# Kernel optimization log

Measured on AMD Instinct MI355X. Metric: run time of the kernel, lower is better.

Reference implementation:

```python
import jax, jax.numpy as jnp
import numpy as np

BLOCK_SIZE = 256
N_EMBD = 256
HEAD_SIZE = 64


def setup_inputs() -> dict:
    key = jax.random.key(0)
    k1, k2, k3, k4, k5 = jax.random.split(key, 5)
    B, T = 256, 256
    x = jax.random.normal(k1, (B, T, N_EMBD), dtype=jnp.float32)
    # nn.Linear(n_embd, head_size, bias=False) weights, stored as [in, out] for x @ W
    s = 1.0 / np.sqrt(N_EMBD)
    Wk = jax.random.uniform(k2, (N_EMBD, HEAD_SIZE), minval=-s, maxval=s, dtype=jnp.float32)
    Wq = jax.random.uniform(k3, (N_EMBD, HEAD_SIZE), minval=-s, maxval=s, dtype=jnp.float32)
    Wv = jax.random.uniform(k4, (N_EMBD, HEAD_SIZE), minval=-s, maxval=s, dtype=jnp.float32)
    rel_pos_embedding = 0.02 * jax.random.normal(k5, (2 * BLOCK_SIZE - 1, HEAD_SIZE), dtype=jnp.float32)
    return {"x": x, "Wk": Wk, "Wq": Wq, "Wv": Wv, "rel_pos_embedding": rel_pos_embedding}


def reference(x, Wk, Wq, Wv, rel_pos_embedding):
    B, T, C = x.shape
    H = Wk.shape[-1]
    k = x @ Wk  # [B,T,H]
    q = x @ Wq  # [B,T,H]
    v = x @ Wv  # [B,T,H]
    # content scores (scaled); note: position scores are NOT scaled, matching original
    content = jnp.einsum('bth,bsh->bts', q, k) * (H ** -0.5)  # [B,T,T]
    # relative position indices: j - i + (block_size - 1)
    idx = jnp.arange(T)[None, :] - jnp.arange(T)[:, None] + (BLOCK_SIZE - 1)  # [T,T]
    rel_emb = rel_pos_embedding[idx]  # [T,T,H]
    position = jnp.einsum('bth,tsh->bts', q, rel_emb)  # [B,T,T]
    wei = content + position
    causal = jnp.tril(jnp.ones((T, T), dtype=bool))
    wei = jnp.where(causal[None, :, :], wei, -jnp.inf)
    wei = jax.nn.softmax(wei, axis=-1)
    # dropout omitted (eval mode / deterministic reference)
    out = jnp.einsum('bts,bsh->bth', wei, v)  # [B,T,H]
    return out
```

## Files before the change

kernel.cpp:

```cpp
#include <hip/hip_runtime.h>

#define BB 256
#define TT 256
#define CC 256
#define HH 64

typedef _Float16 half8 __attribute__((ext_vector_type(8)));
typedef _Float16 half4 __attribute__((ext_vector_type(4)));
typedef __fp16 fp16x2 __attribute__((ext_vector_type(2)));
typedef float floatx4 __attribute__((ext_vector_type(4)));

__global__ __launch_bounds__(256) void prep(
    const float* __restrict__ rpe,
    const float* __restrict__ Wk, const float* __restrict__ Wq, const float* __restrict__ Wv,
    _Float16* __restrict__ rpeh, _Float16* __restrict__ WT)
{
    const int bid = blockIdx.x, tid = threadIdx.x;
    if (bid < 64) {
        const int i = bid * 256 + tid;
        rpeh[i] = (_Float16)rpe[i];
    } else {
        const int wsel = (bid - 64) >> 6;
        const int n    = (bid - 64) & 63;
        const float* W = wsel == 0 ? Wk : (wsel == 1 ? Wq : Wv);
        WT[(size_t)(wsel * 64 + n) * 256 + tid] = (_Float16)W[tid * HH + n];
    }
}

__global__ __launch_bounds__(1024, 4) void fused(
    const float* __restrict__ x, const _Float16* __restrict__ WT,
    const _Float16* __restrict__ rpeh,
    _Float16* __restrict__ qh, _Float16* __restrict__ kh, _Float16* __restrict__ vTh,
    float* __restrict__ out)
{
    __shared__ __align__(16) unsigned char ldsbuf[16 * 16 * 264 * 2];
    _Float16* wt = (_Float16*)ldsbuf;

    const int tid  = threadIdx.x;
    const int b    = blockIdx.x;
    const int w    = tid >> 6;
    const int lane = tid & 63;
    const int quad = lane >> 4;
    const int l    = lane & 15;

    union H8 { half8 v; fp16x2 p[4]; };

#pragma unroll
    for (int i = tid; i < 192 * 32; i += 1024) {
        const int row = i >> 5;
        const int g   = i & 31;
        const int pg  = g ^ (row & 31);
        *(half8*)&wt[row * 256 + pg * 8] = *(const half8*)(WT + (size_t)row * 256 + g * 8);
    }
    __syncthreads();

    {
        const int row0 = b * 256 + w * 16;
        floatx4 acc[12];
#pragma unroll
        for (int nt = 0; nt < 12; ++nt) acc[nt] = (floatx4){0.f, 0.f, 0.f, 0.f};

        const float4* xg = reinterpret_cast<const float4*>(x);

#pragma unroll
        for (int kk = 0; kk < 8; ++kk) {
            const size_t base = (size_t)(row0 + l) * 64 + kk * 8 + quad * 2;
            const float4 alo = xg[base], ahi = xg[base + 1];
            H8 u;
            u.p[0] = __builtin_amdgcn_cvt_pkrtz(alo.x, alo.y);
            u.p[1] = __builtin_amdgcn_cvt_pkrtz(alo.z, alo.w);
            u.p[2] = __builtin_amdgcn_cvt_pkrtz(ahi.x, ahi.y);
            u.p[3] = __builtin_amdgcn_cvt_pkrtz(ahi.z, ahi.w);

#pragma unroll
            for (int nt = 0; nt < 12; ++nt) {
                const int row = nt * 16 + l;
                const int pg  = (kk * 4 + quad) ^ (row & 31);
                const half8 bf = *(const half8*)&wt[row * 256 + pg * 8];
                acc[nt] = __builtin_amdgcn_mfma_f32_16x16x32_f16(u.v, bf, acc[nt], 0, 0, 0);
            }
        }

        const int trw = w * 16;
#pragma unroll
        for (int nt = 0; nt < 4; ++nt) {
#pragma unroll
            for (int r = 0; r < 4; ++r) {
                const size_t row = (size_t)row0 + quad * 4 + r;
                kh[row * HH + nt * 16 + l] = (_Float16)(acc[nt][r] * 0.125f);
                qh[row * HH + nt * 16 + l] = (_Float16)acc[nt + 4][r];
            }
            half4 vv;
            vv[0] = (_Float16)acc[nt + 8][0];
            vv[1] = (_Float16)acc[nt + 8][1];
            vv[2] = (_Float16)acc[nt + 8][2];
            vv[3] = (_Float16)acc[nt + 8][3];
            *(half4*)(vTh + ((size_t)b * HH + nt * 16 + l) * TT + trw + quad * 4) = vv;
        }
    }
    __syncthreads();

    _Float16* wh = (_Float16*)ldsbuf + w * (16 * 264);
    {
        const int tile  = w;
        const int tw    = tile * 16;
        const int stmax = tile;
        const int cmax  = tile >> 1;
        const int dtmin = 15 - tile;

        const _Float16* qp = qh + (size_t)(b * TT + tw + l) * HH + quad * 8;
        const half8 qf0 = *(const half8*)qp;
        const half8 qf1 = *(const half8*)(qp + 32);

#pragma unroll
        for (int dt = 0; dt < 16; ++dt) {
            if (dt >= dtmin) {
                const _Float16* rp = rpeh + (size_t)(dt * 16 + l) * HH + quad * 8;
                const half8 bf0 = *(const half8*)rp;
                const half8 bf1 = *(const half8*)(rp + 32);
                floatx4 z = {0.f, 0.f, 0.f, 0.f};
                z = __builtin_amdgcn_mfma_f32_16x16x32_f16(qf0, bf0, z, 0, 0, 0);
                const floatx4 pacc = __builtin_amdgcn_mfma_f32_16x16x32_f16(qf1, bf1, z, 0, 0, 0);
                if (dt == dtmin) {
#pragma unroll
                    for (int r = 0; r < 4; ++r) {
                        const int row = quad * 4 + r;
                        const int s   = l + row - 15;
                        if (s >= 0) wh[row * 264 + s] = (_Float16)pacc[r];
                    }
                } else {
#pragma unroll
                    for (int r = 0; r < 4; ++r) {
                        const int row = quad * 4 + r;
                        const int s   = dt * 16 + l + tw + row - 255;
                        wh[row * 264 + s] = (_Float16)pacc[r];
                    }
                }
            }
        }

        floatx4 sacc[16];
#pragma unroll
        for (int st = 0; st < 16; ++st) {
            if (st <= stmax) {
                const _Float16* kp = kh + (size_t)(b * TT + st * 16 + l) * HH + quad * 8;
                const half8 kf0 = *(const half8*)kp;
                const half8 kf1 = *(const half8*)(kp + 32);
                floatx4 z = {0.f, 0.f, 0.f, 0.f};
                z = __builtin_amdgcn_mfma_f32_16x16x32_f16(qf0, kf0, z, 0, 0, 0);
                sacc[st] = __builtin_amdgcn_mfma_f32_16x16x32_f16(qf1, kf1, z, 0, 0, 0);
            }
        }

        float sums[4] = {0.f, 0.f, 0.f, 0.f};
#pragma unroll
        for (int st = 0; st < 16; ++st) {
            if (st < stmax) {
                const int s = l + 16 * st;
#pragma unroll
                for (int r = 0; r < 4; ++r) {
                    const int row = quad * 4 + r;
                    const float e = __expf(sacc[st][r] + (float)wh[row * 264 + s]);
                    sums[r] += e;
                    wh[row * 264 + s] = (_Float16)e;
                }
            }
        }
        {
            const int s = l + 16 * stmax;
#pragma unroll
            for (int r = 0; r < 4; ++r) {
                const int row = quad * 4 + r;
                float e = 0.f;
                if (l <= row) e = __expf(sacc[stmax][r] + (float)wh[row * 264 + s]);
                sums[r] += e;
                wh[row * 264 + s] = (_Float16)e;
            }
        }
        if ((tile & 1) == 0) {
            const int s = l + 16 * (stmax + 1);
#pragma unroll
            for (int r = 0; r < 4; ++r) wh[(quad * 4 + r) * 264 + s] = (_Float16)0.f;
        }

        float inv_r[4];
#pragma unroll
        for (int r = 0; r < 4; ++r) {
            float sum = sums[r];
            sum += __shfl_xor(sum, 1);
            sum += __shfl_xor(sum, 2);
            sum += __shfl_xor(sum, 4);
            sum += __shfl_xor(sum, 8);
            inv_r[r] = 1.0f / sum;
        }

        floatx4 oacc[4] = {{0.f,0.f,0.f,0.f},{0.f,0.f,0.f,0.f},
                           {0.f,0.f,0.f,0.f},{0.f,0.f,0.f,0.f}};
#pragma unroll
        for (int c = 0; c < 8; ++c) {
            if (c <= cmax) {
                const half8 af = *(const half8*)&wh[l * 264 + c * 32 + quad * 8];
#pragma unroll
                for (int ht = 0; ht < 4; ++ht) {
                    const half8 vf = *(const half8*)(vTh +
                        ((size_t)b * HH + ht * 16 + l) * TT + c * 32 + quad * 8);
                    oacc[ht] = __builtin_amdgcn_mfma_f32_16x16x32_f16(af, vf, oacc[ht], 0, 0, 0);
                }
            }
        }

#pragma unroll
        for (int ht = 0; ht < 4; ++ht) {
#pragma unroll
            for (int r = 0; r < 4; ++r) {
                const int t = tw + quad * 4 + r;
                out[(size_t)(b * TT + t) * HH + ht * 16 + l] = oacc[ht][r] * inv_r[r];
            }
        }
    }
}

extern "C" void kernel_launch(void* const* d_in, const int* in_sizes, int n_in,
                              void* d_out, int out_size, void* d_ws, size_t ws_size,
                              hipStream_t stream) {
    const float* x   = (const float*)d_in[0];
    const float* Wk  = (const float*)d_in[1];
    const float* Wq  = (const float*)d_in[2];
    const float* Wv  = (const float*)d_in[3];
    const float* rpe = (const float*)d_in[4];
    float* out = (float*)d_out;

    const size_t NQ = (size_t)BB * TT * HH;
    _Float16* qh   = (_Float16*)d_ws;
    _Float16* kh   = qh + NQ;
    _Float16* vTh  = kh + NQ;
    _Float16* rpeh = vTh + NQ;
    _Float16* WT   = rpeh + 256 * HH;

    prep<<<dim3(256), dim3(256), 0, stream>>>(rpe, Wk, Wq, Wv, rpeh, WT);
    fused<<<dim3(BB), dim3(1024), 0, stream>>>(x, WT, rpeh, qh, kh, vTh, out);
}
```

Baseline: 146.0 us.

## Keep K, V^T and Q in LDS instead of round-tripping through global workspace

The fused kernel no longer writes q/k/vT to a global workspace and reads them back. K and V^T now go into shared memory, and each wave passes its Q fragment through its own score slot. The weight staging is split into two 128-column halves in a pooled LDS region. That region is then reused for per-wave score buffers with triangular, variable widths, so the larger LDS footprint still fits. This removes global write and read traffic and its latency, at the cost of about 150KB of LDS per block and an extra barrier in the projection phase.

```diff
diff --git a/kernel.cpp b/kernel.cpp
--- a/kernel.cpp
+++ b/kernel.cpp
@@ -27,14 +27,25 @@
     }
 }
 
+__device__ __forceinline__ int slot_width(int w) {
+    const int j = w >> 1;
+    return (j < 2) ? 72 : (32 * j + 40);
+}
+__device__ __forceinline__ int slot_off(int w) {
+    const int j = w >> 1;
+    const int V = (j < 2) ? 72 : (32 * j + 40);
+    const int S = (j == 0) ? 0 : (j == 1) ? 72 : (16 * j * j + 24 * j + 32);
+    return 32 * S + (w & 1) * 16 * V;
+}
+
 __global__ __launch_bounds__(1024, 4) void fused(
     const float* __restrict__ x, const _Float16* __restrict__ WT,
-    const _Float16* __restrict__ rpeh,
-    _Float16* __restrict__ qh, _Float16* __restrict__ kh, _Float16* __restrict__ vTh,
-    float* __restrict__ out)
+    const _Float16* __restrict__ rpeh, float* __restrict__ out)
 {
-    __shared__ __align__(16) unsigned char ldsbuf[16 * 16 * 264 * 2];
-    _Float16* wt = (_Float16*)ldsbuf;
+    __shared__ _Float16 lds[75264];
+    _Float16* Klds = lds;
+    _Float16* VT   = lds + 18432;
+    _Float16* pool = lds + 35328;
 
     const int tid  = threadIdx.x;
     const int b    = blockIdx.x;
@@ -44,178 +55,186 @@
     const int l    = lane & 15;
 
     union H8 { half8 v; fp16x2 p[4]; };
-
-#pragma unroll
-    for (int i = tid; i < 192 * 32; i += 1024) {
-        const int row = i >> 5;
-        const int g   = i & 31;
-        const int pg  = g ^ (row & 31);
-        *(half8*)&wt[row * 256 + pg * 8] = *(const half8*)(WT + (size_t)row * 256 + g * 8);
-    }
-    __syncthreads();
+    const float4* xg = reinterpret_cast<const float4*>(x);
+    const int row0g = b * 256 + w * 16;
+
+    floatx4 acc[12];
+#pragma unroll
+    for (int nt = 0; nt < 12; ++nt) acc[nt] = (floatx4){0.f, 0.f, 0.f, 0.f};
+
+#pragma unroll
+    for (int c = 0; c < 2; ++c) {
+#pragma unroll
+        for (int i = 0; i < 3; ++i) {
+            const int gi  = tid + i * 1024;
+            const int row = gi >> 4;
+            const int g   = gi & 15;
+            *(half8*)&pool[row * 136 + g * 8] =
+                *(const half8*)(WT + (size_t)row * 256 + c * 128 + g * 8);
+        }
+        __syncthreads();
+
+        float4 xa[4][2];
+#pragma unroll
+        for (int kk = 0; kk < 4; ++kk) {
+            const size_t base = (size_t)(row0g + l) * 64 + c * 32 + kk * 8 + quad * 2;
+            xa[kk][0] = xg[base];
+            xa[kk][1] = xg[base + 1];
+        }
+#pragma unroll
+        for (int kk = 0; kk < 4; ++kk) {
+            H8 u;
+            u.p[0] = __builtin_amdgcn_cvt_pkrtz(xa[kk][0].x, xa[kk][0].y);
+            u.p[1] = __builtin_amdgcn_cvt_pkrtz(xa[kk][0].z, xa[kk][0].w);
+            u.p[2] = __builtin_amdgcn_cvt_pkrtz(xa[kk][1].x, xa[kk][1].y);
+            u.p[3] = __builtin_amdgcn_cvt_pkrtz(xa[kk][1].z, xa[kk][1].w);
+#pragma unroll
+            for (int nt = 0; nt < 12; ++nt) {
+                const half8 bf = *(const half8*)&pool[(nt * 16 + l) * 136 + kk * 32 + quad * 8];
+                acc[nt] = __builtin_amdgcn_mfma_f32_16x16x32_f16(u.v, bf, acc[nt], 0, 0, 0);
+            }
+        }
+        __syncthreads();
+    }
 
     {
-        const int row0 = b * 256 + w * 16;
-        floatx4 acc[12];
-#pragma unroll
-        for (int nt = 0; nt < 12; ++nt) acc[nt] = (floatx4){0.f, 0.f, 0.f, 0.f};
-
-        const float4* xg = reinterpret_cast<const float4*>(x);
-
-#pragma unroll
-        for (int kk = 0; kk < 8; ++kk) {
-            const size_t base = (size_t)(row0 + l) * 64 + kk * 8 + quad * 2;
-            const float4 alo = xg[base], ahi = xg[base + 1];
-            H8 u;
-            u.p[0] = __builtin_amdgcn_cvt_pkrtz(alo.x, alo.y);
-            u.p[1] = __builtin_amdgcn_cvt_pkrtz(alo.z, alo.w);
-            u.p[2] = __builtin_amdgcn_cvt_pkrtz(ahi.x, ahi.y);
-            u.p[3] = __builtin_amdgcn_cvt_pkrtz(ahi.z, ahi.w);
-
-#pragma unroll
-            for (int nt = 0; nt < 12; ++nt) {
-                const int row = nt * 16 + l;
-                const int pg  = (kk * 4 + quad) ^ (row & 31);
-                const half8 bf = *(const half8*)&wt[row * 256 + pg * 8];
-                acc[nt] = __builtin_amdgcn_mfma_f32_16x16x32_f16(u.v, bf, acc[nt], 0, 0, 0);
-            }
-        }
-
         const int trw = w * 16;
 #pragma unroll
         for (int nt = 0; nt < 4; ++nt) {
 #pragma unroll
-            for (int r = 0; r < 4; ++r) {
-                const size_t row = (size_t)row0 + quad * 4 + r;
-                kh[row * HH + nt * 16 + l] = (_Float16)(acc[nt][r] * 0.125f);
-                qh[row * HH + nt * 16 + l] = (_Float16)acc[nt + 4][r];
-            }
+            for (int r = 0; r < 4; ++r)
+                Klds[(trw + quad * 4 + r) * 72 + nt * 16 + l] = (_Float16)(acc[nt][r] * 0.125f);
             half4 vv;
             vv[0] = (_Float16)acc[nt + 8][0];
             vv[1] = (_Float16)acc[nt + 8][1];
             vv[2] = (_Float16)acc[nt + 8][2];
             vv[3] = (_Float16)acc[nt + 8][3];
-            *(half4*)(vTh + ((size_t)b * HH + nt * 16 + l) * TT + trw + quad * 4) = vv;
+            *(half4*)&VT[(nt * 16 + l) * 264 + trw + quad * 4] = vv;
         }
     }
     __syncthreads();
 
-    _Float16* wh = (_Float16*)ldsbuf + w * (16 * 264);
+    _Float16* wh = pool + slot_off(w);
+    const int Vw = slot_width(w);
+    const int tile  = w;
+    const int tw    = tile * 16;
+    const int stmax = tile;
+    const int cmax  = tile >> 1;
+    const int dtmin = 15 - tile;
+
+    half8 qf0, qf1;
     {
-        const int tile  = w;
-        const int tw    = tile * 16;
-        const int stmax = tile;
-        const int cmax  = tile >> 1;
-        const int dtmin = 15 - tile;
-
-        const _Float16* qp = qh + (size_t)(b * TT + tw + l) * HH + quad * 8;
-        const half8 qf0 = *(const half8*)qp;
-        const half8 qf1 = *(const half8*)(qp + 32);
-
-#pragma unroll
-        for (int dt = 0; dt < 16; ++dt) {
-            if (dt >= dtmin) {
-                const _Float16* rp = rpeh + (size_t)(dt * 16 + l) * HH + quad * 8;
-                const half8 bf0 = *(const half8*)rp;
-                const half8 bf1 = *(const half8*)(rp + 32);
-                floatx4 z = {0.f, 0.f, 0.f, 0.f};
-                z = __builtin_amdgcn_mfma_f32_16x16x32_f16(qf0, bf0, z, 0, 0, 0);
-                const floatx4 pacc = __builtin_amdgcn_mfma_f32_16x16x32_f16(qf1, bf1, z, 0, 0, 0);
-                if (dt == dtmin) {
-#pragma unroll
-                    for (int r = 0; r < 4; ++r) {
-                        const int row = quad * 4 + r;
-                        const int s   = l + row - 15;
-                        if (s >= 0) wh[row * 264 + s] = (_Float16)pacc[r];
-                    }
-                } else {
-#pragma unroll
-                    for (int r = 0; r < 4; ++r) {
-                        const int row = quad * 4 + r;
-                        const int s   = dt * 16 + l + tw + row - 255;
-                        wh[row * 264 + s] = (_Float16)pacc[r];
-                    }
-                }
-            }
-        }
-
-        floatx4 sacc[16];
-#pragma unroll
-        for (int st = 0; st < 16; ++st) {
-            if (st <= stmax) {
-                const _Float16* kp = kh + (size_t)(b * TT + st * 16 + l) * HH + quad * 8;
-                const half8 kf0 = *(const half8*)kp;
-                const half8 kf1 = *(const half8*)(kp + 32);
-                floatx4 z = {0.f, 0.f, 0.f, 0.f};
-                z = __builtin_amdgcn_mfma_f32_16x16x32_f16(qf0, kf0, z, 0, 0, 0);
-                sacc[st] = __builtin_amdgcn_mfma_f32_16x16x32_f16(qf1, kf1, z, 0, 0, 0);
-            }
-        }
-
-        float sums[4] = {0.f, 0.f, 0.f, 0.f};
-#pragma unroll
-        for (int st = 0; st < 16; ++st) {
-            if (st < stmax) {
-                const int s = l + 16 * st;
+#pragma unroll
+        for (int nt = 0; nt < 4; ++nt)
+#pragma unroll
+            for (int r = 0; r < 4; ++r)
+                wh[(quad * 4 + r) * Vw + nt * 16 + l] = (_Float16)acc[nt + 4][r];
+        qf0 = *(const half8*)&wh[l * Vw + quad * 8];
+        qf1 = *(const half8*)&wh[l * Vw + 32 + quad * 8];
+    }
+
+#pragma unroll
+    for (int dt = 0; dt < 16; ++dt) {
+        if (dt >= dtmin) {
+            const _Float16* rp = rpeh + (size_t)(dt * 16 + l) * HH + quad * 8;
+            const half8 bf0 = *(const half8*)rp;
+            const half8 bf1 = *(const half8*)(rp + 32);
+            floatx4 z = {0.f, 0.f, 0.f, 0.f};
+            z = __builtin_amdgcn_mfma_f32_16x16x32_f16(qf0, bf0, z, 0, 0, 0);
+            const floatx4 pacc = __builtin_amdgcn_mfma_f32_16x16x32_f16(qf1, bf1, z, 0, 0, 0);
+            if (dt == dtmin) {
 #pragma unroll
                 for (int r = 0; r < 4; ++r) {
                     const int row = quad * 4 + r;
-                    const float e = __expf(sacc[st][r] + (float)wh[row * 264 + s]);
-                    sums[r] += e;
-                    wh[row * 264 + s] = (_Float16)e;
+                    const int s   = l + row - 15;
+                    if (s >= 0) wh[row * Vw + s] = (_Float16)pacc[r];
                 }
-            }
-        }
-        {
-            const int s = l + 16 * stmax;
+            } else {
+#pragma unroll
+                for (int r = 0; r < 4; ++r) {
+                    const int row = quad * 4 + r;
+                    const int s   = dt * 16 + l + tw + row - 255;
+                    wh[row * Vw + s] = (_Float16)pacc[r];
+                }
+            }
+        }
+    }
+
+    floatx4 sacc[16];
+#pragma unroll
+    for (int st = 0; st < 16; ++st) {
+        if (st <= stmax) {
+            const _Float16* kp = &Klds[(st * 16 + l) * 72 + quad * 8];
+            const half8 kf0 = *(const half8*)kp;
+            const half8 kf1 = *(const half8*)(kp + 32);
+            floatx4 z = {0.f, 0.f, 0.f, 0.f};
+            z = __builtin_amdgcn_mfma_f32_16x16x32_f16(qf0, kf0, z, 0, 0, 0);
+            sacc[st] = __builtin_amdgcn_mfma_f32_16x16x32_f16(qf1, kf1, z, 0, 0, 0);
+        }
+    }
+
+    float sums[4] = {0.f, 0.f, 0.f, 0.f};
+#pragma unroll
+    for (int st = 0; st < 16; ++st) {
+        if (st < stmax) {
+            const int s = l + 16 * st;
 #pragma unroll
             for (int r = 0; r < 4; ++r) {
                 const int row = quad * 4 + r;
-                float e = 0.f;
-                if (l <= row) e = __expf(sacc[stmax][r] + (float)wh[row * 264 + s]);
+                const float e = __expf(sacc[st][r] + (float)wh[row * Vw + s]);
                 sums[r] += e;
-                wh[row * 264 + s] = (_Float16)e;
-            }
-        }
-        if ((tile & 1) == 0) {
-            const int s = l + 16 * (stmax + 1);
-#pragma unroll
-            for (int r = 0; r < 4; ++r) wh[(quad * 4 + r) * 264 + s] = (_Float16)0.f;
-        }
-
-        float inv_r[4];
+                wh[row * Vw + s] = (_Float16)e;
+            }
+        }
+    }
+    {
+        const int s = l + 16 * stmax;
 #pragma unroll
         for (int r = 0; r < 4; ++r) {
-            float sum = sums[r];
-            sum += __shfl_xor(sum, 1);
-            sum += __shfl_xor(sum, 2);
-            sum += __shfl_xor(sum, 4);
-            sum += __shfl_xor(sum, 8);
-            inv_r[r] = 1.0f / sum;
-        }
-
-        floatx4 oacc[4] = {{0.f,0.f,0.f,0.f},{0.f,0.f,0.f,0.f},
-                           {0.f,0.f,0.f,0.f},{0.f,0.f,0.f,0.f}};
-#pragma unroll
-        for (int c = 0; c < 8; ++c) {
-            if (c <= cmax) {
-                const half8 af = *(const half8*)&wh[l * 264 + c * 32 + quad * 8];
-#pragma unroll
-                for (int ht = 0; ht < 4; ++ht) {
-                    const half8 vf = *(const half8*)(vTh +
-                        ((size_t)b * HH + ht * 16 + l) * TT + c * 32 + quad * 8);
-                    oacc[ht] = __builtin_amdgcn_mfma_f32_16x16x32_f16(af, vf, oacc[ht], 0, 0, 0);
-                }
-            }
-        }
-
-#pragma unroll
-        for (int ht = 0; ht < 4; ++ht) {
-#pragma unroll
-            for (int r = 0; r < 4; ++r) {
-                const int t = tw + quad * 4 + r;
-                out[(size_t)(b * TT + t) * HH + ht * 16 + l] = oacc[ht][r] * inv_r[r];
-            }
+            const int row = quad * 4 + r;
+            float e = 0.f;
+            if (l <= row) e = __expf(sacc[stmax][r] + (float)wh[row * Vw + s]);
+            sums[r] += e;
+            wh[row * Vw + s] = (_Float16)e;
+        }
+    }
+    if ((tile & 1) == 0) {
+        const int s = l + 16 * (stmax + 1);
+#pragma unroll
+        for (int r = 0; r < 4; ++r) wh[(quad * 4 + r) * Vw + s] = (_Float16)0.f;
+    }
+
+    float inv_r[4];
+#pragma unroll
+    for (int r = 0; r < 4; ++r) {
+        float sum = sums[r];
+        sum += __shfl_xor(sum, 1);
+        sum += __shfl_xor(sum, 2);
+        sum += __shfl_xor(sum, 4);
+        sum += __shfl_xor(sum, 8);
+        inv_r[r] = 1.0f / sum;
+    }
+
+    floatx4 oacc[4] = {{0.f,0.f,0.f,0.f},{0.f,0.f,0.f,0.f},
+                       {0.f,0.f,0.f,0.f},{0.f,0.f,0.f,0.f}};
+#pragma unroll
+    for (int c = 0; c < 8; ++c) {
+        if (c <= cmax) {
+            const half8 af = *(const half8*)&wh[l * Vw + c * 32 + quad * 8];
+#pragma unroll
+            for (int ht = 0; ht < 4; ++ht) {
+                const half8 vf = *(const half8*)&VT[(ht * 16 + l) * 264 + c * 32 + quad * 8];
+                oacc[ht] = __builtin_amdgcn_mfma_f32_16x16x32_f16(af, vf, oacc[ht], 0, 0, 0);
+            }
+        }
+    }
+
+#pragma unroll
+    for (int ht = 0; ht < 4; ++ht) {
+#pragma unroll
+        for (int r = 0; r < 4; ++r) {
+            const int t = tw + quad * 4 + r;
+            out[(size_t)(b * TT + t) * HH + ht * 16 + l] = oacc[ht][r] * inv_r[r];
         }
     }
 }
@@ -230,13 +249,9 @@
     const float* rpe = (const float*)d_in[4];
     float* out = (float*)d_out;
 
-    const size_t NQ = (size_t)BB * TT * HH;
-    _Float16* qh   = (_Float16*)d_ws;
-    _Float16* kh   = qh + NQ;
-    _Float16* vTh  = kh + NQ;
-    _Float16* rpeh = vTh + NQ;
+    _Float16* rpeh = (_Float16*)d_ws;
     _Float16* WT   = rpeh + 256 * HH;
 
     prep<<<dim3(256), dim3(256), 0, stream>>>(rpe, Wk, Wq, Wv, rpeh, WT);
-    fused<<<dim3(BB), dim3(1024), 0, stream>>>(x, WT, rpeh, qh, kh, vTh, out);
-}
+    fused<<<dim3(BB), dim3(1024), 0, stream>>>(x, WT, rpeh, out);
+}
```

After: 132.3 us. -9.4%, faster.
